# Kernel tuning notes

Measured on AMD Instinct MI355X. Metric: run time of the kernel, lower is better.

The kernel has to match this reference:

```python
import jax, jax.numpy as jnp
import numpy as np

EPS = 1e-05


def setup_inputs() -> dict:
    key = jax.random.key(0)
    kx, = jax.random.split(key, 1)
    B, C, T = 8, 512, 8192
    x = jax.random.normal(kx, (B, C, T), dtype=jnp.float32)
    weight = jnp.ones((1, C, 1), dtype=jnp.float32)
    bias = jnp.zeros((1, C, 1), dtype=jnp.float32)
    return {"x": x, "weight": weight, "bias": bias}


def reference(x, weight, bias):
    # x: [B, C, T]; causal (running) per-channel mean/var over time.
    T = x.shape[-1]
    count = jnp.arange(1, T + 1, dtype=x.dtype)  # [T], broadcasts over B,C
    cumsum = jnp.cumsum(x, axis=-1)
    cumsum_sq = jnp.cumsum(x * x, axis=-1)
    mean = cumsum / count
    var = cumsum_sq / count - mean * mean
    x_norm = (x - mean) * jax.lax.rsqrt(var + EPS)
    return x_norm * weight + bias
```

## Files before the change

kernel.cpp:

```cpp
#include <hip/hip_runtime.h>
#include <math.h>

#define EPS 1e-5f
#define T_LEN 8192
#define WAVES_PER_BLOCK 4

template<int CTRL, int RM>
__device__ __forceinline__ float dpp_add(float x) {
    int sh = __builtin_amdgcn_update_dpp(0, __float_as_int(x),
                                         CTRL, RM, 0xF, false);
    return x + __int_as_float(sh);
}

__device__ __forceinline__ float wave64_incl_scan(float x) {
    x = dpp_add<0x111, 0xF>(x);
    x = dpp_add<0x112, 0xF>(x);
    x = dpp_add<0x114, 0xF>(x);
    x = dpp_add<0x118, 0xF>(x);
    x = dpp_add<0x142, 0xA>(x);
    x = dpp_add<0x143, 0xC>(x);
    return x;
}

__global__ __launch_bounds__(256) void causal_ln_kernel(
    const float* __restrict__ x,
    const float* __restrict__ weight,
    const float* __restrict__ bias,
    float* __restrict__ out,
    int C)
{
    const int t    = threadIdx.x;
    const int lane = t & 63;
    const int wid  = t >> 6;
    const int row  = blockIdx.x * WAVES_PER_BLOCK + wid;

    const float wv = weight[row % C];
    const float bv = bias[row % C];

    const float4* xg = (const float4*)(x   + (long long)row * T_LEN);
    float4*       og = (float4*)(out + (long long)row * T_LEN);

    float4 buf[4];
#pragma unroll
    for (int j = 0; j < 4; ++j)
        buf[j] = xg[j * 64 + lane];

    float off1 = 0.f, off2 = 0.f;

#pragma unroll
    for (int c = 0; c < 32; ++c) {
        float4 cur = buf[c & 3];
        if (c + 4 < 32)
            buf[c & 3] = xg[(c + 4) * 64 + lane];

        float cb = (float)((c * 64 + lane) * 4);
        float rcv[4];
#pragma unroll
        for (int i = 0; i < 4; ++i)
            rcv[i] = __builtin_amdgcn_rcpf(cb + (float)(i + 1));

        float s  = cur.x + cur.y + cur.z + cur.w;
        float s2 = cur.x * cur.x + cur.y * cur.y
                 + cur.z * cur.z + cur.w * cur.w;

        float ws  = wave64_incl_scan(s);
        float ws2 = wave64_incl_scan(s2);

        float run  = off1 + (ws  - s);
        float run2 = off2 + (ws2 - s2);

        float xs[4] = {cur.x, cur.y, cur.z, cur.w};
#pragma unroll
        for (int i = 0; i < 4; ++i) {
            float xi = xs[i];
            run  += xi;
            run2 += xi * xi;
            float mean = run * rcv[i];
            float var  = fmaxf(run2 * rcv[i] - mean * mean, 0.f);
            float rinv = __builtin_amdgcn_rsqf(var + EPS);
            xs[i] = (xi - mean) * rinv * wv + bv;
        }
        og[c * 64 + lane] = make_float4(xs[0], xs[1], xs[2], xs[3]);

        off1 += __int_as_float(__builtin_amdgcn_readlane(__float_as_int(ws),  63));
        off2 += __int_as_float(__builtin_amdgcn_readlane(__float_as_int(ws2), 63));
    }
}

extern "C" void kernel_launch(void* const* d_in, const int* in_sizes, int n_in,
                              void* d_out, int out_size, void* d_ws, size_t ws_size,
                              hipStream_t stream) {
    const float* x      = (const float*)d_in[0];
    const float* weight = (const float*)d_in[1];
    const float* bias   = (const float*)d_in[2];
    float* out          = (float*)d_out;

    const int C = in_sizes[1];
    const int T = 8192;
    const int rows = in_sizes[0] / T;

    dim3 grid(rows / WAVES_PER_BLOCK), block(64 * WAVES_PER_BLOCK);
    hipLaunchKernelGGL(causal_ln_kernel, grid, block, 0, stream,
                       x, weight, bias, out, C);
}
```

Before: 240.5 us.

## Process each row with a 1024-thread block using a cross-wave LDS scan

Instead of one wave walking a whole 8192-element row serially in 32 chunks, each row now gets a 1024-thread block where every thread handles 8 contiguous elements. Per-wave inclusive scans are combined through shared memory after a block barrier, which removes the long serial dependency chain of readlane offsets. This gives more parallelism and memory-level parallelism per row, at the cost of a __syncthreads and a 16-wave block that may limit occupancy and register headroom. Each thread now loads two adjacent float4s, so consecutive lanes read 32-byte strided addresses rather than contiguous 16-byte ones.

```diff
diff --git a/kernel.cpp b/kernel.cpp
--- a/kernel.cpp
+++ b/kernel.cpp
@@ -3,7 +3,6 @@
 
 #define EPS 1e-5f
 #define T_LEN 8192
-#define WAVES_PER_BLOCK 4
 
 template<int CTRL, int RM>
 __device__ __forceinline__ float dpp_add(float x) {
@@ -22,69 +21,67 @@
     return x;
 }
 
-__global__ __launch_bounds__(256) void causal_ln_kernel(
+__global__ __launch_bounds__(1024, 8) void causal_ln_kernel(
     const float* __restrict__ x,
     const float* __restrict__ weight,
     const float* __restrict__ bias,
     float* __restrict__ out,
     int C)
 {
+    __shared__ float2 wtot[16];
+
     const int t    = threadIdx.x;
     const int lane = t & 63;
     const int wid  = t >> 6;
-    const int row  = blockIdx.x * WAVES_PER_BLOCK + wid;
+    const int row  = blockIdx.x;
 
     const float wv = weight[row % C];
     const float bv = bias[row % C];
 
-    const float4* xg = (const float4*)(x   + (long long)row * T_LEN);
-    float4*       og = (float4*)(out + (long long)row * T_LEN);
+    const float4* xg = (const float4*)(x + (long long)row * T_LEN);
+    float4 v0 = xg[2 * t];
+    float4 v1 = xg[2 * t + 1];
 
-    float4 buf[4];
+    float rcv[8];
 #pragma unroll
-    for (int j = 0; j < 4; ++j)
-        buf[j] = xg[j * 64 + lane];
+    for (int i = 0; i < 8; ++i)
+        rcv[i] = __builtin_amdgcn_rcpf((float)(8 * t + i + 1));
+
+    float xs[8] = {v0.x, v0.y, v0.z, v0.w, v1.x, v1.y, v1.z, v1.w};
+
+    float s = 0.f, s2 = 0.f;
+#pragma unroll
+    for (int i = 0; i < 8; ++i) { s += xs[i]; s2 += xs[i] * xs[i]; }
+
+    float ws  = wave64_incl_scan(s);
+    float ws2 = wave64_incl_scan(s2);
+
+    if (lane == 63) wtot[wid] = make_float2(ws, ws2);
+    __syncthreads();
 
     float off1 = 0.f, off2 = 0.f;
+#pragma unroll
+    for (int w = 0; w < 15; ++w) {
+        if (w < wid) { off1 += wtot[w].x; off2 += wtot[w].y; }
+    }
+
+    float run  = off1 + (ws  - s);
+    float run2 = off2 + (ws2 - s2);
 
 #pragma unroll
-    for (int c = 0; c < 32; ++c) {
-        float4 cur = buf[c & 3];
-        if (c + 4 < 32)
-            buf[c & 3] = xg[(c + 4) * 64 + lane];
+    for (int i = 0; i < 8; ++i) {
+        float xi = xs[i];
+        run  += xi;
+        run2 += xi * xi;
+        float mean = run * rcv[i];
+        float var  = fmaxf(run2 * rcv[i] - mean * mean, 0.f);
+        float rinv = __builtin_amdgcn_rsqf(var + EPS);
+        xs[i] = (xi - mean) * rinv * wv + bv;
+    }
 
-        float cb = (float)((c * 64 + lane) * 4);
-        float rcv[4];
-#pragma unroll
-        for (int i = 0; i < 4; ++i)
-            rcv[i] = __builtin_amdgcn_rcpf(cb + (float)(i + 1));
-
-        float s  = cur.x + cur.y + cur.z + cur.w;
-        float s2 = cur.x * cur.x + cur.y * cur.y
-                 + cur.z * cur.z + cur.w * cur.w;
-
-        float ws  = wave64_incl_scan(s);
-        float ws2 = wave64_incl_scan(s2);
-
-        float run  = off1 + (ws  - s);
-        float run2 = off2 + (ws2 - s2);
-
-        float xs[4] = {cur.x, cur.y, cur.z, cur.w};
-#pragma unroll
-        for (int i = 0; i < 4; ++i) {
-            float xi = xs[i];
-            run  += xi;
-            run2 += xi * xi;
-            float mean = run * rcv[i];
-            float var  = fmaxf(run2 * rcv[i] - mean * mean, 0.f);
-            float rinv = __builtin_amdgcn_rsqf(var + EPS);
-            xs[i] = (xi - mean) * rinv * wv + bv;
-        }
-        og[c * 64 + lane] = make_float4(xs[0], xs[1], xs[2], xs[3]);
-
-        off1 += __int_as_float(__builtin_amdgcn_readlane(__float_as_int(ws),  63));
-        off2 += __int_as_float(__builtin_amdgcn_readlane(__float_as_int(ws2), 63));
-    }
+    float4* og = (float4*)(out + (long long)row * T_LEN);
+    og[2 * t]     = make_float4(xs[0], xs[1], xs[2], xs[3]);
+    og[2 * t + 1] = make_float4(xs[4], xs[5], xs[6], xs[7]);
 }
 
 extern "C" void kernel_launch(void* const* d_in, const int* in_sizes, int n_in,
@@ -99,7 +96,7 @@
     const int T = 8192;
     const int rows = in_sizes[0] / T;
 
-    dim3 grid(rows / WAVES_PER_BLOCK), block(64 * WAVES_PER_BLOCK);
+    dim3 grid(rows), block(1024);
     hipLaunchKernelGGL(causal_ln_kernel, grid, block, 0, stream,
                        x, weight, bias, out, C);
 }
```

Measured after the change: 233.6 us. 1.03x faster.
